# Performance work log

Measured on AMD Instinct MI355X. Metric: run time of the kernel, lower is better.

## Reference

```python
import jax, jax.numpy as jnp
import numpy as np

N_NODES = 100000
NEG_SLOPE = 0.2  # PyG GATConv default


def _add_self_loops(edge_index, n):
    loop = jnp.arange(n, dtype=edge_index.dtype)
    src = jnp.concatenate([edge_index[0], loop])
    dst = jnp.concatenate([edge_index[1], loop])
    return src, dst


def _gat_conv(x, src, dst, W, a_src, a_dst, b, n):
    h = x @ W                                   # [N, d]
    alpha_src = h @ a_src                        # [N]
    alpha_dst = h @ a_dst                        # [N]
    e = alpha_src[src] + alpha_dst[dst]          # [E]
    e = jnp.where(e >= 0, e, NEG_SLOPE * e)      # LeakyReLU
    # segment softmax over incoming edges of each target node
    m = jax.ops.segment_max(e, dst, num_segments=n)   # every node has a self loop
    ex = jnp.exp(e - m[dst])
    denom = jax.ops.segment_sum(ex, dst, num_segments=n)
    alpha = ex / denom[dst]                      # [E]
    out = jax.ops.segment_sum(h[src] * alpha[:, None], dst, num_segments=n)
    return out + b


def setup_inputs() -> dict:
    key = jax.random.key(0)
    ks = jax.random.split(key, 10)
    num_feat, dim = 14, 16
    E = 3200000
    x = jax.random.normal(ks[0], (N_NODES, num_feat), dtype=jnp.float32)
    edge_index = jax.random.randint(ks[1], (2, E), 0, N_NODES, dtype=jnp.int64)
    s1 = 1.0 / np.sqrt(num_feat)
    s2 = 1.0 / np.sqrt(dim)
    return {
        "x": x,
        "edge_index": edge_index,
        "W1": jax.random.uniform(ks[2], (num_feat, dim), jnp.float32, -s1, s1),
        "a_src1": jax.random.uniform(ks[3], (dim,), jnp.float32, -s2, s2),
        "a_dst1": jax.random.uniform(ks[4], (dim,), jnp.float32, -s2, s2),
        "b1": jnp.zeros((dim,), jnp.float32),
        "W2": jax.random.uniform(ks[5], (dim, dim), jnp.float32, -s2, s2),
        "a_src2": jax.random.uniform(ks[6], (dim,), jnp.float32, -s2, s2),
        "a_dst2": jax.random.uniform(ks[7], (dim,), jnp.float32, -s2, s2),
        "b2": jnp.zeros((dim,), jnp.float32),
    }


def reference(x, edge_index, W1, a_src1, a_dst1, b1, W2, a_src2, a_dst2, b2):
    n = x.shape[0]
    src, dst = _add_self_loops(edge_index, n)
    h = _gat_conv(x, src, dst, W1, a_src1, a_dst1, b1, n)
    h = jax.nn.relu(h)
    # F.dropout in eval mode is identity
    out = _gat_conv(h, src, dst, W2, a_src2, a_dst2, b2, n)
    return out
```

## Files before the change

kernel.cpp:

```cpp
#include <hip/hip_runtime.h>
#include <hip/hip_fp16.h>

static constexpr float SLOPE = 0.2f;

#define NPB 256
#define NBMAX 512
#define CAP 10240
#define EPB 8192

__device__ __forceinline__ unsigned fkey(float f) {
    unsigned u = __float_as_uint(f);
    return (u & 0x80000000u) ? ~u : (u | 0x80000000u);
}
__device__ __forceinline__ float fdekey(unsigned k) {
    unsigned u = (k & 0x80000000u) ? (k & 0x7FFFFFFFu) : ~k;
    return __uint_as_float(u);
}

__device__ __forceinline__ int load_idx(const void* ei, int is64, long long pos) {
    return is64 ? (int)((const long long*)ei)[pos] : ((const int*)ei)[pos];
}

__global__ void __launch_bounds__(1024) bin_kernel(
        const void* __restrict__ ei, int* __restrict__ bfill,
        unsigned int* __restrict__ packed, int e, int nb) {
    __shared__ int hist[NBMAX];
    __shared__ int lbase[NBMAX];
    __shared__ int cur[NBMAX];
    __shared__ unsigned staged[EPB];
    __shared__ unsigned short sbkt[EPB];
    __shared__ int sflag;
    int t = threadIdx.x;
    if (t < 64) {
        unsigned hi = ((const unsigned*)ei)[2 * t + 1];
        unsigned long long b = __ballot(hi != 0u);
        if (t == 0) sflag = (b == 0ull) ? 1 : 0;
    }
    for (int i = t; i < NBMAX; i += 1024) hist[i] = 0;
    __syncthreads();
    int is64 = sflag;
    long long e0 = (long long)blockIdx.x * EPB;
    int cnt = (int)min((long long)EPB, (long long)e - e0);
    int sr[8], dr[8];
#pragma unroll
    for (int r = 0; r < 8; ++r) {
        int i = t + r * 1024;
        dr[r] = -1;
        if (i < cnt) {
            sr[r] = load_idx(ei, is64, e0 + i);
            dr[r] = load_idx(ei, is64, (long long)e + e0 + i);
            atomicAdd(&hist[dr[r] >> 8], 1);
        }
    }
    __syncthreads();
    int v = (t < NBMAX) ? hist[t] : 0;
    if (t < NBMAX) lbase[t] = v;
    __syncthreads();
    for (int off = 1; off < NBMAX; off <<= 1) {
        int y = (t < NBMAX && t >= off) ? lbase[t - off] : 0;
        __syncthreads();
        if (t < NBMAX) lbase[t] += y;
        __syncthreads();
    }
    if (t < NBMAX) {
        lbase[t] -= v;
        cur[t] = lbase[t];
        hist[t] = (v > 0) ? atomicAdd(&bfill[t], v) : 0;
    }
    __syncthreads();
#pragma unroll
    for (int r = 0; r < 8; ++r) {
        if (dr[r] >= 0) {
            int bk = dr[r] >> 8;
            int lp = atomicAdd(&cur[bk], 1);
            staged[lp] = ((unsigned)(dr[r] & 255) << 17) | (unsigned)sr[r];
            sbkt[lp] = (unsigned short)bk;
        }
    }
    __syncthreads();
    for (int i = t; i < cnt; i += 1024) {
        int bk = sbkt[i];
        int within = hist[bk] + (i - lbase[bk]);
        if (within < CAP)
            packed[(long long)bk * CAP + within] = staged[i];
    }
}

__global__ void build_kernel(const unsigned int* __restrict__ packed,
                             const int* __restrict__ bfill,
                             int* __restrict__ offs, int* __restrict__ csr, int n) {
    __shared__ int hist[NPB];
    __shared__ int tmp[NPB];
    __shared__ int cur[NPB];
    __shared__ int red[512];
    int b = blockIdx.x, t = threadIdx.x;
    int ps = 0;
    for (int i = t; i < b; i += 512) ps += min(bfill[i], CAP);
    red[t] = ps;
    __syncthreads();
    for (int off = 256; off > 0; off >>= 1) {
        if (t < off) red[t] += red[t + off];
        __syncthreads();
    }
    int base = red[0];
    if (t < NPB) hist[t] = 0;
    __syncthreads();
    int cnt = min(bfill[b], CAP);
    long long pb = (long long)b * CAP;
    for (int i = t; i < cnt; i += 512)
        atomicAdd(&hist[packed[pb + i] >> 17], 1);
    __syncthreads();
    int v = (t < NPB) ? hist[t] : 0;
    if (t < NPB) tmp[t] = v;
    __syncthreads();
    for (int off = 1; off < NPB; off <<= 1) {
        int y = (t < NPB && t >= off) ? tmp[t - off] : 0;
        __syncthreads();
        if (t < NPB) tmp[t] += y;
        __syncthreads();
    }
    if (t < NPB) {
        int excl = tmp[t] - v;
        cur[t] = excl;
        int node = b * NPB + t;
        if (node <= n) offs[node] = base + excl;
    }
    __syncthreads();
    for (int i = t; i < cnt; i += 512) {
        unsigned p = packed[pb + i];
        int lp = atomicAdd(&cur[p >> 17], 1);
        csr[base + lp] = (int)(p & 0x1FFFF);
    }
}

template <int NF>
__global__ void feat_kernel(const float* __restrict__ x, const float* __restrict__ W,
                            const float* __restrict__ avs, const float* __restrict__ avd,
                            float* __restrict__ h, __half* __restrict__ h16,
                            float* __restrict__ as, float* __restrict__ ad,
                            unsigned* __restrict__ gkey, int n) {
    __shared__ float sW[NF * 16];
    __shared__ float sa[32];
    __shared__ float red[256];
    int t = threadIdx.x;
    if (t < NF * 16) sW[t] = W[t];
    if (t < 16) sa[t] = avs[t];
    else if (t < 32) sa[t] = avd[t - 16];
    __syncthreads();
    int nid = blockIdx.x * blockDim.x + t;
    float s1 = -1e30f;
    if (nid < n) {
        float xi[NF];
#pragma unroll
        for (int f = 0; f < NF; ++f) xi[f] = x[(long long)nid * NF + f];
        float hv[16];
        s1 = 0.f;
        float s2 = 0.f;
#pragma unroll
        for (int k = 0; k < 16; ++k) {
            float acc = 0.f;
#pragma unroll
            for (int f = 0; f < NF; ++f) acc = fmaf(xi[f], sW[f * 16 + k], acc);
            hv[k] = acc;
            s1 = fmaf(acc, sa[k], s1);
            s2 = fmaf(acc, sa[16 + k], s2);
        }
        float4* hp = (float4*)(h + (long long)nid * 16);
        hp[0] = make_float4(hv[0], hv[1], hv[2], hv[3]);
        hp[1] = make_float4(hv[4], hv[5], hv[6], hv[7]);
        hp[2] = make_float4(hv[8], hv[9], hv[10], hv[11]);
        hp[3] = make_float4(hv[12], hv[13], hv[14], hv[15]);
        unsigned u[8];
#pragma unroll
        for (int q = 0; q < 8; ++q) {
            __half2 p2 = __halves2half2(__float2half(hv[2 * q]), __float2half(hv[2 * q + 1]));
            u[q] = *(unsigned*)&p2;
        }
        uint4* hp16 = (uint4*)(h16 + (long long)nid * 16);
        hp16[0] = make_uint4(u[0], u[1], u[2], u[3]);
        hp16[1] = make_uint4(u[4], u[5], u[6], u[7]);
        as[nid] = s1;
        ad[nid] = s2;
    }
    red[t] = s1;
    __syncthreads();
    for (int off = 128; off > 0; off >>= 1) {
        if (t < off) red[t] = fmaxf(red[t], red[t + off]);
        __syncthreads();
    }
    if (t == 0) atomicMax(gkey, fkey(red[0]));
}

__global__ void aggr_kernel(const float* __restrict__ h, const __half* __restrict__ h16,
                            const float* __restrict__ as, const float* __restrict__ ad,
                            const int* __restrict__ offs, const int* __restrict__ csr,
                            const float* __restrict__ bias,
                            const unsigned* __restrict__ gkey,
                            float* __restrict__ out, int n, int do_relu) {
    int t = threadIdx.x;
    int node = blockIdx.x * 16 + (t >> 4);
    int k = t & 15;
    if (node >= n) return;
    int gbase = t & 48;
    float adn = ad[node];
    float gm = fdekey(*gkey) + adn;
    float m = fmaxf(gm, SLOPE * gm);
    float eself = as[node] + adn;
    eself = fmaxf(eself, SLOPE * eself);
    float kb = fminf(7.f, fmaxf(0.f, floorf((m - eself) * 1.44269504f)));
    float cc = (21.f + kb) * 0.69314718f - m;
    float wself = __expf(eself + cc);
    long long acc = (int)(wself * h[(long long)node * 16 + k]);
    long long den = 0;
    int j0 = offs[node], j1 = offs[node + 1];
    for (int jb = j0; jb < j1; jb += 16) {
        int jj = jb + k;
        float w = 0.f;
        int s = 0;
        if (jj < j1) {
            s = csr[jj];
            float e2 = as[s] + adn;
            e2 = fmaxf(e2, SLOPE * e2);
            w = __expf(e2 + cc);
        }
        den += (long long)(int)w;
#pragma unroll
        for (int u = 0; u < 16; ++u) {
            float wu = __shfl(w, gbase + u, 64);
            int su = __shfl(s, gbase + u, 64);
            float hv = __half2float(h16[(long long)su * 16 + k]);
            acc += (long long)(int)(wu * hv);
        }
    }
#pragma unroll
    for (int mask = 1; mask < 16; mask <<= 1)
        den += __shfl_xor(den, mask, 64);
    den += (long long)(int)wself;
    float o = (float)acc / (float)den + bias[k];
    if (do_relu) o = fmaxf(o, 0.f);
    out[(long long)node * 16 + k] = o;
}

extern "C" void kernel_launch(void* const* d_in, const int* in_sizes, int n_in,
                              void* d_out, int out_size, void* d_ws, size_t ws_size,
                              hipStream_t stream) {
    const float* x  = (const float*)d_in[0];
    const void*  ei = d_in[1];
    const float* W1  = (const float*)d_in[2];
    const float* as1 = (const float*)d_in[3];
    const float* ad1 = (const float*)d_in[4];
    const float* b1  = (const float*)d_in[5];
    const float* W2  = (const float*)d_in[6];
    const float* as2 = (const float*)d_in[7];
    const float* ad2 = (const float*)d_in[8];
    const float* b2  = (const float*)d_in[9];
    float* out = (float*)d_out;

    const int n = in_sizes[0] / 14;
    const int e = in_sizes[1] / 2;
    const int nb = (n + NPB - 1) / NPB;

    char* p = (char*)d_ws;
    auto alloc = [&](size_t bytes) {
        char* r = p;
        p += (bytes + 255) & ~(size_t)255;
        return r;
    };
    unsigned* gkeys  = (unsigned*)alloc(256);
    int*      bfill  = (int*)alloc(NBMAX * 4);
    unsigned* packed = (unsigned*)alloc((size_t)nb * CAP * 4);
    int*      offs   = (int*)alloc((size_t)(n + 1) * 4);
    int*      csr    = (int*)alloc((size_t)e * 4);
    float*    h      = (float*)alloc((size_t)n * 16 * 4);
    __half*   h16    = (__half*)alloc((size_t)n * 16 * 2);
    float*    h1     = (float*)alloc((size_t)n * 16 * 4);
    float*    asb    = (float*)alloc((size_t)n * 4);
    float*    adb    = (float*)alloc((size_t)n * 4);

    hipMemsetAsync(gkeys, 0, 256 + NBMAX * 4, stream);
    bin_kernel<<<(e + EPB - 1) / EPB, 1024, 0, stream>>>(ei, bfill, packed, e, nb);
    build_kernel<<<nb, 512, 0, stream>>>(packed, bfill, offs, csr, n);

    feat_kernel<14><<<(n + 255) / 256, 256, 0, stream>>>(x, W1, as1, ad1, h, h16, asb, adb, gkeys + 0, n);
    aggr_kernel<<<(n + 15) / 16, 256, 0, stream>>>(h, h16, asb, adb, offs, csr, b1, gkeys + 0, h1, n, 1);
    feat_kernel<16><<<(n + 255) / 256, 256, 0, stream>>>(h1, W2, as2, ad2, h, h16, asb, adb, gkeys + 1, n);
    aggr_kernel<<<(n + 15) / 16, 256, 0, stream>>>(h, h16, asb, adb, offs, csr, b2, gkeys + 1, out, n, 0);
}
```

Baseline: 148.0 us.

## Use 32 lanes per node in aggregation and vectorize edge binning loads

The aggregation kernel now gives each node 32 lanes instead of 16. The two 16-lane halves each gather alternate edges, and their integer accumulators are combined with one xor-shuffle at the end. The bin kernel drops to 512 threads and 4096 edges per block, and it loads eight contiguous int32 indices per thread with uint4 vector reads when indices are 32-bit. Together these aim to increase memory-level parallelism for the gathers and the index reads. In exchange, each wave now covers half as many nodes, the extra reduction adds shuffles, and the number of bin blocks doubles, which means more atomics on the global bucket-fill counters.

```diff
diff --git a/kernel.cpp b/kernel.cpp
--- a/kernel.cpp
+++ b/kernel.cpp
@@ -6,7 +6,7 @@
 #define NPB 256
 #define NBMAX 512
 #define CAP 10240
-#define EPB 8192
+#define EPB 4096
 
 __device__ __forceinline__ unsigned fkey(float f) {
     unsigned u = __float_as_uint(f);
@@ -21,7 +21,7 @@
     return is64 ? (int)((const long long*)ei)[pos] : ((const int*)ei)[pos];
 }
 
-__global__ void __launch_bounds__(1024) bin_kernel(
+__global__ void __launch_bounds__(512) bin_kernel(
         const void* __restrict__ ei, int* __restrict__ bfill,
         unsigned int* __restrict__ packed, int e, int nb) {
     __shared__ int hist[NBMAX];
@@ -36,22 +36,34 @@
         unsigned long long b = __ballot(hi != 0u);
         if (t == 0) sflag = (b == 0ull) ? 1 : 0;
     }
-    for (int i = t; i < NBMAX; i += 1024) hist[i] = 0;
+    if (t < NBMAX) hist[t] = 0;
     __syncthreads();
     int is64 = sflag;
     long long e0 = (long long)blockIdx.x * EPB;
     int cnt = (int)min((long long)EPB, (long long)e - e0);
     int sr[8], dr[8];
-#pragma unroll
-    for (int r = 0; r < 8; ++r) {
-        int i = t + r * 1024;
-        dr[r] = -1;
-        if (i < cnt) {
-            sr[r] = load_idx(ei, is64, e0 + i);
-            dr[r] = load_idx(ei, is64, (long long)e + e0 + i);
-            atomicAdd(&hist[dr[r] >> 8], 1);
-        }
-    }
+    if (!is64 && t * 8 + 7 < cnt) {
+        const uint4* ps = (const uint4*)((const int*)ei + e0) + t * 2;
+        const uint4* pd = (const uint4*)((const int*)ei + e + e0) + t * 2;
+        uint4 s0 = ps[0], s1 = ps[1], d0 = pd[0], d1 = pd[1];
+        sr[0] = s0.x; sr[1] = s0.y; sr[2] = s0.z; sr[3] = s0.w;
+        sr[4] = s1.x; sr[5] = s1.y; sr[6] = s1.z; sr[7] = s1.w;
+        dr[0] = d0.x; dr[1] = d0.y; dr[2] = d0.z; dr[3] = d0.w;
+        dr[4] = d1.x; dr[5] = d1.y; dr[6] = d1.z; dr[7] = d1.w;
+    } else {
+#pragma unroll
+        for (int r = 0; r < 8; ++r) {
+            int i = t * 8 + r;
+            dr[r] = -1;
+            if (i < cnt) {
+                sr[r] = load_idx(ei, is64, e0 + i);
+                dr[r] = load_idx(ei, is64, (long long)e + e0 + i);
+            }
+        }
+    }
+#pragma unroll
+    for (int r = 0; r < 8; ++r)
+        if (dr[r] >= 0) atomicAdd(&hist[dr[r] >> 8], 1);
     __syncthreads();
     int v = (t < NBMAX) ? hist[t] : 0;
     if (t < NBMAX) lbase[t] = v;
@@ -78,7 +90,7 @@
         }
     }
     __syncthreads();
-    for (int i = t; i < cnt; i += 1024) {
+    for (int i = t; i < cnt; i += 512) {
         int bk = sbkt[i];
         int within = hist[bk] + (i - lbase[bk]);
         if (within < CAP)
@@ -198,10 +210,11 @@
                             const unsigned* __restrict__ gkey,
                             float* __restrict__ out, int n, int do_relu) {
     int t = threadIdx.x;
-    int node = blockIdx.x * 16 + (t >> 4);
+    int node = blockIdx.x * 8 + (t >> 5);
     int k = t & 15;
+    int half = (t >> 4) & 1;
+    int gbase = t & 32;
     if (node >= n) return;
-    int gbase = t & 48;
     float adn = ad[node];
     float gm = fdekey(*gkey) + adn;
     float m = fmaxf(gm, SLOPE * gm);
@@ -210,11 +223,11 @@
     float kb = fminf(7.f, fmaxf(0.f, floorf((m - eself) * 1.44269504f)));
     float cc = (21.f + kb) * 0.69314718f - m;
     float wself = __expf(eself + cc);
-    long long acc = (int)(wself * h[(long long)node * 16 + k]);
+    long long acc = half ? 0ll : (long long)(int)(wself * h[(long long)node * 16 + k]);
     long long den = 0;
     int j0 = offs[node], j1 = offs[node + 1];
-    for (int jb = j0; jb < j1; jb += 16) {
-        int jj = jb + k;
+    for (int jb = j0; jb < j1; jb += 32) {
+        int jj = jb + (t & 31);
         float w = 0.f;
         int s = 0;
         if (jj < j1) {
@@ -226,19 +239,23 @@
         den += (long long)(int)w;
 #pragma unroll
         for (int u = 0; u < 16; ++u) {
-            float wu = __shfl(w, gbase + u, 64);
-            int su = __shfl(s, gbase + u, 64);
+            int src_lane = gbase + 2 * u + half;
+            float wu = __shfl(w, src_lane, 64);
+            int su = __shfl(s, src_lane, 64);
             float hv = __half2float(h16[(long long)su * 16 + k]);
             acc += (long long)(int)(wu * hv);
         }
     }
-#pragma unroll
-    for (int mask = 1; mask < 16; mask <<= 1)
+    acc += __shfl_xor(acc, 16, 64);
+#pragma unroll
+    for (int mask = 1; mask < 32; mask <<= 1)
         den += __shfl_xor(den, mask, 64);
     den += (long long)(int)wself;
-    float o = (float)acc / (float)den + bias[k];
-    if (do_relu) o = fmaxf(o, 0.f);
-    out[(long long)node * 16 + k] = o;
+    if (half == 0) {
+        float o = (float)acc / (float)den + bias[k];
+        if (do_relu) o = fmaxf(o, 0.f);
+        out[(long long)node * 16 + k] = o;
+    }
 }
 
 extern "C" void kernel_launch(void* const* d_in, const int* in_sizes, int n_in,
@@ -278,11 +295,11 @@
     float*    adb    = (float*)alloc((size_t)n * 4);
 
     hipMemsetAsync(gkeys, 0, 256 + NBMAX * 4, stream);
-    bin_kernel<<<(e + EPB - 1) / EPB, 1024, 0, stream>>>(ei, bfill, packed, e, nb);
+    bin_kernel<<<(e + EPB - 1) / EPB, 512, 0, stream>>>(ei, bfill, packed, e, nb);
     build_kernel<<<nb, 512, 0, stream>>>(packed, bfill, offs, csr, n);
 
     feat_kernel<14><<<(n + 255) / 256, 256, 0, stream>>>(x, W1, as1, ad1, h, h16, asb, adb, gkeys + 0, n);
-    aggr_kernel<<<(n + 15) / 16, 256, 0, stream>>>(h, h16, asb, adb, offs, csr, b1, gkeys + 0, h1, n, 1);
+    aggr_kernel<<<(n + 7) / 8, 256, 0, stream>>>(h, h16, asb, adb, offs, csr, b1, gkeys + 0, h1, n, 1);
     feat_kernel<16><<<(n + 255) / 256, 256, 0, stream>>>(h1, W2, as2, ad2, h, h16, asb, adb, gkeys + 1, n);
-    aggr_kernel<<<(n + 15) / 16, 256, 0, stream>>>(h, h16, asb, adb, offs, csr, b2, gkeys + 1, out, n, 0);
-}
+    aggr_kernel<<<(n + 7) / 8, 256, 0, stream>>>(h, h16, asb, adb, offs, csr, b2, gkeys + 1, out, n, 0);
+}
```

New measurement: 166.3 us. 1.12x slower.
